# Kernel optimization log

Measured on AMD Instinct MI355X. Metric: run time of the kernel, lower is better.

Reference implementation:

```python
import jax, jax.numpy as jnp
import numpy as np

HIDDEN = 1024
D_INNER = 2048
DT_RANK = 64
STATE = 16
KCONV = 4


def setup_inputs() -> dict:
    key = jax.random.key(0)
    ks = jax.random.split(key, 9)
    s = lambda k, shape, sc=0.02: jax.random.normal(k, shape, dtype=jnp.float32) * sc
    return {
        "x": jax.random.normal(ks[0], (2, 1024, HIDDEN), dtype=jnp.float32),
        "in_proj_w": s(ks[1], (2 * D_INNER, HIDDEN)),
        "conv_w": s(ks[2], (D_INNER, 1, KCONV), 0.2),
        "conv_b": s(ks[3], (D_INNER,), 0.1),
        "x_proj_w": s(ks[4], (DT_RANK + 2 * STATE, D_INNER)),
        "dt_proj_w": s(ks[5], (D_INNER, DT_RANK), 0.1),
        "dt_proj_b": s(ks[6], (D_INNER,), 0.1),
        "A_log": s(ks[7], (D_INNER, STATE), 0.5),
        "out_proj_w": s(ks[8], (HIDDEN, D_INNER)),
    }


def _selective_scan(u, delta, A, B, C):
    # u, delta: (b,l,d); A: (d,n); B, C: (b,l,n)
    deltaA = jnp.exp(delta[..., None] * A)               # (b,l,d,n)
    dBu = (delta * u)[..., None] * B[:, :, None, :]      # (b,l,d,n)
    # scan over time axis; carry h: (b,d,n)
    deltaA_t = jnp.moveaxis(deltaA, 1, 0)                # (l,b,d,n)
    dBu_t = jnp.moveaxis(dBu, 1, 0)                      # (l,b,d,n)
    C_t = jnp.moveaxis(C, 1, 0)                          # (l,b,n)

    def step(h, inp):
        dA_i, dBu_i, C_i = inp
        h = dA_i * h + dBu_i
        y = jnp.einsum('bdn,bn->bd', h, C_i)
        return h, y

    h0 = jnp.zeros(u.shape[:1] + u.shape[2:] + (A.shape[1],), dtype=u.dtype)
    _, ys = jax.lax.scan(step, h0, (deltaA_t, dBu_t, C_t))
    return jnp.moveaxis(ys, 0, 1)                        # (b,l,d)


def reference(x, in_proj_w, conv_w, conv_b, x_proj_w, dt_proj_w, dt_proj_b, A_log, out_proj_w):
    b, l, _ = x.shape
    xr = x @ in_proj_w.T                                 # (b,l,2*d_inner)
    xs, res = jnp.split(xr, 2, axis=-1)
    # causal depthwise conv1d: pad left k-1 (matches padding=k-1 then [:l])
    xc = jnp.moveaxis(xs, 1, 2)                          # (b,d,l)
    xc = jax.lax.conv_general_dilated(
        xc, conv_w, window_strides=(1,), padding=[(KCONV - 1, 0)],
        feature_group_count=D_INNER,
        dimension_numbers=('NCH', 'OIH', 'NCH'))
    xc = xc + conv_b[None, :, None]
    xs = jnp.moveaxis(xc, 2, 1)                          # (b,l,d)
    xs = jax.nn.silu(xs)
    x_dbl = xs @ x_proj_w.T                              # (b,l,dt_rank+2n)
    dt, B, C = jnp.split(x_dbl, [DT_RANK, DT_RANK + STATE], axis=-1)
    delta = jax.nn.softplus(dt @ dt_proj_w.T + dt_proj_b)
    A = -jnp.exp(A_log.astype(jnp.float32))
    y = _selective_scan(xs, delta, A, B, C)
    y = y * jax.nn.silu(res)
    return y @ out_proj_w.T
```

## Files before the change

### kernel.cpp

```cpp
#include <hip/hip_runtime.h>

typedef unsigned short u16;
typedef __bf16 bf16x8 __attribute__((ext_vector_type(8)));
typedef float f32x4 __attribute__((ext_vector_type(4)));

__device__ inline float bf2f(u16 u) {
    unsigned int x = ((unsigned int)u) << 16;
    return __builtin_bit_cast(float, x);
}
__device__ inline u16 f2bf(float f) {
    unsigned int x = __builtin_bit_cast(unsigned int, f);
    return (u16)((x + 0x7FFFu + ((x >> 16) & 1u)) >> 16);
}
__device__ inline float sigm(float v) { return 1.f / (1.f + __expf(-v)); }

__device__ __forceinline__ void gload16(const void* g, void* l) {
    __builtin_amdgcn_global_load_lds(
        (const __attribute__((address_space(1))) void*)g,
        (__attribute__((address_space(3))) void*)l, 16, 0, 0);
}

__device__ inline uint4 pack8(const float* p) {
    const float4* q = (const float4*)p;
    float4 a = q[0], b = q[1];
    union { u16 h[8]; uint4 v; } u;
    u.h[0] = f2bf(a.x); u.h[1] = f2bf(a.y); u.h[2] = f2bf(a.z); u.h[3] = f2bf(a.w);
    u.h[4] = f2bf(b.x); u.h[5] = f2bf(b.y); u.h[6] = f2bf(b.z); u.h[7] = f2bf(b.w);
    return u.v;
}

__global__ __launch_bounds__(256)
void cvt_front(const float* __restrict__ x, const float* __restrict__ inw,
               const float* __restrict__ xpw, const float* __restrict__ convw,
               u16* __restrict__ x_bf, u16* __restrict__ inw_bf,
               u16* __restrict__ xpw_bf, float* __restrict__ wt)
{
    int bk = blockIdx.x, tid = threadIdx.x;
    if (bk < 1024) {
        int i = bk * 256 + tid;
        ((uint4*)x_bf)[i] = pack8(x + (size_t)i * 8);
    } else if (bk < 3072) {
        int i = (bk - 1024) * 256 + tid;
        ((uint4*)inw_bf)[i] = pack8(inw + (size_t)i * 8);
    } else if (bk < 3200) {
        int i = (bk - 3072) * 256 + tid;
        int row = (i * 8) >> 11;
        ((uint4*)xpw_bf)[i] = (row < 96) ? pack8(xpw + (size_t)row * 2048 + ((i * 8) & 2047))
                                         : make_uint4(0u, 0u, 0u, 0u);
    } else {
        int i = (bk - 3200) * 256 + tid;
        wt[(i & 3) * 2048 + (i >> 2)] = convw[i];
    }
}

__global__ __launch_bounds__(256)
void cvt_bf16(const float* __restrict__ in, u16* __restrict__ out)
{
    int i = blockIdx.x * 256 + threadIdx.x;
    ((uint4*)out)[i] = pack8(in + (size_t)i * 8);
}

template<int EPI, bool OUTF32>
__global__ __launch_bounds__(256, 2)
void gemm2(const u16* __restrict__ A, int lda,
           const u16* __restrict__ B, int ldb,
           void* __restrict__ Cout, int ldc,
           int N, int ksplit, size_t zElems,
           const float* __restrict__ bias)
{
    __shared__ u16 sA[128][64];
    __shared__ u16 sB[128][64];

    const int tid  = threadIdx.x;
    const int lane = tid & 63;
    const int wave = tid >> 6;

    int nxy = gridDim.x * gridDim.y;
    int id  = blockIdx.y * gridDim.x + blockIdx.x;
    int bx, by;
    if ((nxy & 7) == 0) {
        int cpx = nxy >> 3;
        int swz = (id & 7) * cpx + (id >> 3);
        bx = swz % gridDim.x;
        by = swz / gridDim.x;
    } else { bx = blockIdx.x; by = blockIdx.y; }

    const int wm = (wave >> 1) * 64;
    const int wn = (wave & 1) * 64;
    const int m0 = by * 128;
    const int n0 = bx * 128;
    const int lm = lane & 15;
    const int g  = lane >> 4;
    const int k0 = blockIdx.z * ksplit;

    const int rr = lane >> 3;
    const int sl = lane & 7;
    const int xsl = sl ^ rr;
    const u16* gA = A + (size_t)(m0 + wave * 8 + rr) * lda + k0 + xsl * 8;
    const u16* gB = B + (size_t)(n0 + wave * 8 + rr) * ldb + k0 + xsl * 8;
    const int ldsRow = (wave * 8) * 128;

    f32x4 acc[4][4] = {};

    for (int kb = 0; kb < ksplit; kb += 64) {
        #pragma unroll
        for (int c = 0; c < 4; ++c) {
            gload16(gA + (size_t)c * 32 * lda + kb, (char*)sA + c * 4096 + ldsRow);
            gload16(gB + (size_t)c * 32 * ldb + kb, (char*)sB + c * 4096 + ldsRow);
        }
        __syncthreads();

        bf16x8 af[2][4], bfr[2][4];
        #pragma unroll
        for (int h = 0; h < 2; ++h) {
            #pragma unroll
            for (int i = 0; i < 4; ++i) {
                int ra = wm + i * 16 + lm;
                int rb = wn + i * 16 + lm;
                int chunk = (((h << 2) | g) ^ (lm & 7)) << 4;
                af[h][i]  = *(const bf16x8*)((const char*)sA + ra * 128 + chunk);
                bfr[h][i] = *(const bf16x8*)((const char*)sB + rb * 128 + chunk);
            }
        }
        #pragma unroll
        for (int h = 0; h < 2; ++h)
            #pragma unroll
            for (int i = 0; i < 4; ++i)
                #pragma unroll
                for (int j = 0; j < 4; ++j)
                    acc[i][j] = __builtin_amdgcn_mfma_f32_16x16x32_bf16(af[h][i], bfr[h][j], acc[i][j], 0, 0, 0);
        __syncthreads();
    }

    #pragma unroll
    for (int i = 0; i < 4; ++i) {
        int crow = m0 + wm + i * 16 + ((lane >> 4) << 2);
        #pragma unroll
        for (int j = 0; j < 4; ++j) {
            int ccol = n0 + wn + j * 16 + lm;
            if (ccol < N) {
                #pragma unroll
                for (int r = 0; r < 4; ++r) {
                    float v = acc[i][j][r];
                    if (EPI == 2 && ccol >= 2048) v *= sigm(v);
                    size_t off = (size_t)blockIdx.z * zElems + (size_t)(crow + r) * ldc + ccol;
                    if (OUTF32) ((float*)Cout)[off] = v;
                    else        ((u16*)Cout)[off]   = f2bf(v);
                }
            }
        }
    }
}

__global__ __launch_bounds__(256)
void dt_delta(const u16* __restrict__ xdbl, const float* __restrict__ dtw,
              const float* __restrict__ bias, u16* __restrict__ out)
{
    const int tid = threadIdx.x;
    const int d   = blockIdx.x * 256 + tid;
    const int t0  = blockIdx.y * 16;

    __shared__ float s_x[16][64];

    if (tid < 128) {
        int tok = tid >> 3, ch = tid & 7;
        uint4 v = *(const uint4*)&xdbl[(size_t)(t0 + tok) * 96 + ch * 8];
        const u16* h = (const u16*)&v;
        #pragma unroll
        for (int e = 0; e < 8; ++e) s_x[tok][ch * 8 + e] = bf2f(h[e]);
    }

    float w[64];
    {
        const float4* wp = (const float4*)(dtw + (size_t)d * 64);
        #pragma unroll
        for (int q = 0; q < 16; ++q) {
            float4 v = wp[q];
            w[q * 4 + 0] = v.x; w[q * 4 + 1] = v.y;
            w[q * 4 + 2] = v.z; w[q * 4 + 3] = v.w;
        }
    }
    const float bd = bias[d];
    __syncthreads();

    for (int tok = 0; tok < 16; ++tok) {
        float a0 = bd, a1 = 0.f, a2 = 0.f, a3 = 0.f;
        const float4* xv4 = (const float4*)s_x[tok];
        #pragma unroll
        for (int q = 0; q < 16; ++q) {
            float4 xv = xv4[q];
            a0 = fmaf(w[q * 4 + 0], xv.x, a0);
            a1 = fmaf(w[q * 4 + 1], xv.y, a1);
            a2 = fmaf(w[q * 4 + 2], xv.z, a2);
            a3 = fmaf(w[q * 4 + 3], xv.w, a3);
        }
        float v = (a0 + a1) + (a2 + a3);
        v = (v > 20.f) ? v : log1pf(__expf(v));
        out[(size_t)(t0 + tok) * 4096 + d] = f2bf(v);
    }
}

__global__ __launch_bounds__(256)
void reduce96(const float* __restrict__ splits, u16* __restrict__ xdbl)
{
    int i = blockIdx.x * 256 + threadIdx.x;
    float acc = 0.f;
    #pragma unroll
    for (int z = 0; z < 8; ++z) acc += splits[(size_t)z * 196608 + i];
    xdbl[i] = f2bf(acc);
}

__global__ __launch_bounds__(256)
void reduce_out(const u16* __restrict__ parts, float* __restrict__ out)
{
    int i = blockIdx.x * 256 + threadIdx.x;
    float acc[8] = {};
    #pragma unroll
    for (int z = 0; z < 4; ++z) {
        uint4 v = ((const uint4*)(parts + (size_t)z * 2097152))[i];
        const u16* h = (const u16*)&v;
        #pragma unroll
        for (int e = 0; e < 8; ++e) acc[e] += bf2f(h[e]);
    }
    float4* o = (float4*)(out + (size_t)i * 8);
    o[0] = make_float4(acc[0], acc[1], acc[2], acc[3]);
    o[1] = make_float4(acc[4], acc[5], acc[6], acc[7]);
}

__global__ __launch_bounds__(256)
void conv_silu(const u16* __restrict__ xr, const float* __restrict__ wt,
               const float* __restrict__ bias, u16* __restrict__ xs)
{
    int gi = blockIdx.x * 256 + threadIdx.x;
    int d  = (gi & 255) * 8;
    int t  = (gi >> 8) & 1023;
    int b  = gi >> 18;
    const u16* base = xr + (size_t)b * 4194304 + d;
    float acc[8];
    {
        const float4* bp = (const float4*)(bias + d);
        float4 b0 = bp[0], b1 = bp[1];
        acc[0]=b0.x; acc[1]=b0.y; acc[2]=b0.z; acc[3]=b0.w;
        acc[4]=b1.x; acc[5]=b1.y; acc[6]=b1.z; acc[7]=b1.w;
    }
    #pragma unroll
    for (int j = 0; j < 4; ++j) {
        int ti = t - 3 + j;
        if (ti >= 0) {
            uint4 v = *(const uint4*)(base + (size_t)ti * 4096);
            const u16* h = (const u16*)&v;
            const float4* wp = (const float4*)(wt + j * 2048 + d);
            float4 w0 = wp[0], w1 = wp[1];
            float w8[8] = {w0.x, w0.y, w0.z, w0.w, w1.x, w1.y, w1.z, w1.w};
            #pragma unroll
            for (int e = 0; e < 8; ++e) acc[e] = fmaf(w8[e], bf2f(h[e]), acc[e]);
        }
    }
    union { u16 h[8]; uint4 v; } o;
    #pragma unroll
    for (int e = 0; e < 8; ++e) { float v = acc[e]; o.h[e] = f2bf(v * sigm(v)); }
    ((uint4*)xs)[gi] = o.v;
}

template<int PHC>
__global__ __launch_bounds__(256)
void scan_chunk(const u16* __restrict__ deltag, u16* __restrict__ xsg,
                const u16* __restrict__ xdbl, const float* __restrict__ A_log,
                const u16* __restrict__ xr, float* __restrict__ summ,
                float* __restrict__ ssum)
{
    const int tid = threadIdx.x;
    const int d0 = blockIdx.x * 256;
    const int c  = blockIdx.y;
    const int b  = blockIdx.z;
    const int d  = d0 + tid;
    const int tok0 = b * 1024 + c * 32;

    __shared__ u16 s_del[32][256];
    __shared__ u16 s_uu[32][256];
    __shared__ u16 s_bc[32][32];
    __shared__ u16 s_res[PHC ? 32 : 1][PHC ? 256 : 1];
    __shared__ u16 s_y[PHC ? 32 : 1][PHC ? 256 : 1];

    for (int i = tid; i < 1024; i += 256) {
        int tl = i >> 5, v = i & 31;
        size_t tok = (size_t)(tok0 + tl);
        *(uint4*)&s_del[tl][v * 8] = *(const uint4*)&deltag[tok * 4096 + d0 + v * 8];
        *(uint4*)&s_uu[tl][v * 8]  = *(const uint4*)&xsg[tok * 2048 + d0 + v * 8];
        if (PHC)
            *(uint4*)&s_res[tl][v * 8] = *(const uint4*)&xr[tok * 4096 + 2048 + d0 + v * 8];
    }
    for (int i = tid; i < 1024; i += 256) {
        int tl = i >> 5, j = i & 31;
        s_bc[tl][j] = xdbl[(size_t)(tok0 + tl) * 96 + 64 + j];
    }

    float Ar[16], h[16];
    {
        const float4* Ap = (const float4*)(A_log + (size_t)d * 16);
        #pragma unroll
        for (int q = 0; q < 4; ++q) {
            float4 a = Ap[q];
            Ar[q * 4 + 0] = -__expf(a.x); Ar[q * 4 + 1] = -__expf(a.y);
            Ar[q * 4 + 2] = -__expf(a.z); Ar[q * 4 + 3] = -__expf(a.w);
        }
    }
    if (PHC) {
        const float4* hp = (const float4*)&summ[((size_t)(b * 32 + c) * 2048 + d) * 16];
        #pragma unroll
        for (int q = 0; q < 4; ++q) {
            float4 v = hp[q];
            h[q * 4 + 0] = v.x; h[q * 4 + 1] = v.y; h[q * 4 + 2] = v.z; h[q * 4 + 3] = v.w;
        }
    } else {
        #pragma unroll
        for (int n = 0; n < 16; ++n) h[n] = 0.f;
    }
    __syncthreads();

    float S = 0.f;
    #pragma unroll 4
    for (int tl = 0; tl < 32; ++tl) {
        float dlt = bf2f(s_del[tl][tid]);
        float du = dlt * bf2f(s_uu[tl][tid]);
        if (!PHC) S += dlt;
        #pragma unroll
        for (int n = 0; n < 16; ++n)
            h[n] = fmaf(__expf(dlt * Ar[n]), h[n], du * bf2f(s_bc[tl][n]));
        if (PHC) {
            float y = 0.f;
            #pragma unroll
            for (int n = 0; n < 16; ++n)
                y = fmaf(h[n], bf2f(s_bc[tl][16 + n]), y);
            s_y[tl][tid] = f2bf(y * bf2f(s_res[tl][tid]));
        }
    }

    if (!PHC) {
        float4* bp = (float4*)&summ[((size_t)(b * 32 + c) * 2048 + d) * 16];
        #pragma unroll
        for (int q = 0; q < 4; ++q)
            bp[q] = make_float4(h[q * 4], h[q * 4 + 1], h[q * 4 + 2], h[q * 4 + 3]);
        ssum[(size_t)(b * 32 + c) * 2048 + d] = S;
    } else {
        __syncthreads();
        for (int i = tid; i < 1024; i += 256) {
            int tl = i >> 5, v = i & 31;
            *(uint4*)&xsg[(size_t)(tok0 + tl) * 2048 + d0 + v * 8] = *(uint4*)&s_y[tl][v * 8];
        }
    }
}

__global__ __launch_bounds__(256)
void scan_phaseB(float* __restrict__ summ, const float* __restrict__ ssum,
                 const float* __restrict__ A_log)
{
    int g = blockIdx.x * 256 + threadIdx.x;
    int n = g & 15;
    int d = (g >> 4) & 2047;
    int b = g >> 15;
    float An = -__expf(A_log[(size_t)d * 16 + n]);
    float h = 0.f;
    for (int c = 0; c < 32; ++c) {
        size_t idx = ((size_t)(b * 32 + c) * 2048 + d) * 16 + n;
        float bc = summ[idx];
        float Sc = ssum[(size_t)(b * 32 + c) * 2048 + d];
        summ[idx] = h;
        h = fmaf(__expf(An * Sc), h, bc);
    }
}

__global__ void sentinel_kernel(float* out, float v) { out[0] = v; }

extern "C" void kernel_launch(void* const* d_in, const int* in_sizes, int n_in,
                              void* d_out, int out_size, void* d_ws, size_t ws_size,
                              hipStream_t stream)
{
    const float* x         = (const float*)d_in[0];
    const float* in_w      = (const float*)d_in[1];
    const float* conv_w    = (const float*)d_in[2];
    const float* conv_b    = (const float*)d_in[3];
    const float* xproj_w   = (const float*)d_in[4];
    const float* dtproj_w  = (const float*)d_in[5];
    const float* dtproj_b  = (const float*)d_in[6];
    const float* A_log     = (const float*)d_in[7];
    const float* outproj_w = (const float*)d_in[8];
    float* out = (float*)d_out;

    static const int EXP[9] = {2097152, 4194304, 8192, 2048, 196608, 131072, 2048, 32768, 2097152};
    int bad = -1;
    if (n_in != 9) bad = 9;
    else { for (int i = 0; i < 9; ++i) if (in_sizes[i] != EXP[i]) { bad = i; break; } }
    if (bad < 0 && out_size != 2097152) bad = 10;
    if (bad < 0 && ws_size < 34734080u) bad = 11;
    if (bad >= 0) {
        sentinel_kernel<<<1, 1, 0, stream>>>(out, 131072.f * (1.f + (float)bad / 16.f));
        return;
    }

    char* ws = (char*)d_ws;
    u16*   xr      = (u16*)(ws);
    u16*   xs      = (u16*)(ws + 16777216);
    u16*   xdbl    = (u16*)(ws + 25165824);
    char*  R       = ws + 25559040;
    u16*   x_bf    = xs;
    u16*   inw_bf  = (u16*)(R);
    u16*   xpw_bf  = (u16*)(R + 8388608);
    float* wt      = (float*)(R + 8912896);
    float* splits  = (float*)(R);
    float* summ    = (float*)(R);
    float* ssum    = (float*)(R + 8388608);
    u16*   opw_bf  = (u16*)(R);
    u16*   oparts  = xr;

    cvt_front<<<3232, 256, 0, stream>>>(x, in_w, xproj_w, conv_w,
                                        x_bf, inw_bf, xpw_bf, wt);
    gemm2<2, false><<<dim3(32, 16, 1), 256, 0, stream>>>(
        x_bf, 1024, inw_bf, 1024, xr, 4096, 4096, 1024, 0, nullptr);
    conv_silu<<<2048, 256, 0, stream>>>(xr, wt, conv_b, xs);
    gemm2<0, true><<<dim3(1, 16, 8), 256, 0, stream>>>(
        xs, 2048, xpw_bf, 2048, splits, 96, 96, 256, 196608, nullptr);
    reduce96<<<768, 256, 0, stream>>>(splits, xdbl);
    dt_delta<<<dim3(8, 128), 256, 0, stream>>>(xdbl, dtproj_w, dtproj_b, xr);
    scan_chunk<0><<<dim3(8, 32, 2), 256, 0, stream>>>(xr, xs, xdbl, A_log, xr, summ, ssum);
    scan_phaseB<<<256, 256, 0, stream>>>(summ, ssum, A_log);
    scan_chunk<1><<<dim3(8, 32, 2), 256, 0, stream>>>(xr, xs, xdbl, A_log, xr, summ, ssum);
    cvt_bf16<<<1024, 256, 0, stream>>>(outproj_w, opw_bf);
    gemm2<0, false><<<dim3(8, 16, 4), 256, 0, stream>>>(
        xs, 2048, opw_bf, 2048, oparts, 1024, 1024, 512, 2097152, nullptr);
    reduce_out<<<1024, 256, 0, stream>>>(oparts, out);
}
```

Measured before the change: 244.6 us.

## Fuse out_proj weight conversion into GEMM, use exp2 in scan, batch phaseB loads

Drops the separate cvt_bf16 launch for the out_proj weights: the GEMM now reads the fp32 B operand directly and packs it to bf16 into LDS itself. The scan kernels fold log2(e) into A and call the raw v_exp_f32 instruction instead of __expf, which saves a multiply per exponential. scan_phaseB loads all 32 chunk summaries into registers up front, so the serial chain no longer waits on scattered loads. In exchange, every GEMM tile that touches a weight block converts it again instead of converting once, and phaseB holds more registers.

```diff
diff --git a/kernel.cpp b/kernel.cpp
--- a/kernel.cpp
+++ b/kernel.cpp
@@ -13,6 +13,9 @@
     return (u16)((x + 0x7FFFu + ((x >> 16) & 1u)) >> 16);
 }
 __device__ inline float sigm(float v) { return 1.f / (1.f + __expf(-v)); }
+__device__ inline float ex2(float x) {
+    float r; asm("v_exp_f32 %0, %1" : "=v"(r) : "v"(x)); return r;
+}
 
 __device__ __forceinline__ void gload16(const void* g, void* l) {
     __builtin_amdgcn_global_load_lds(
@@ -53,17 +56,10 @@
     }
 }
 
-__global__ __launch_bounds__(256)
-void cvt_bf16(const float* __restrict__ in, u16* __restrict__ out)
-{
-    int i = blockIdx.x * 256 + threadIdx.x;
-    ((uint4*)out)[i] = pack8(in + (size_t)i * 8);
-}
-
-template<int EPI, bool OUTF32>
+template<int EPI, bool OUTF32, int BSRC>
 __global__ __launch_bounds__(256, 2)
 void gemm2(const u16* __restrict__ A, int lda,
-           const u16* __restrict__ B, int ldb,
+           const void* __restrict__ Bv, int ldb,
            void* __restrict__ Cout, int ldc,
            int N, int ksplit, size_t zElems,
            const float* __restrict__ bias)
@@ -97,7 +93,8 @@
     const int sl = lane & 7;
     const int xsl = sl ^ rr;
     const u16* gA = A + (size_t)(m0 + wave * 8 + rr) * lda + k0 + xsl * 8;
-    const u16* gB = B + (size_t)(n0 + wave * 8 + rr) * ldb + k0 + xsl * 8;
+    const u16*  gB  = (BSRC == 0) ? (const u16*)Bv + (size_t)(n0 + wave * 8 + rr) * ldb + k0 + xsl * 8 : nullptr;
+    const float* gBf = (BSRC == 1) ? (const float*)Bv + (size_t)(n0 + wave * 8 + rr) * ldb + k0 + xsl * 8 : nullptr;
     const int ldsRow = (wave * 8) * 128;
 
     f32x4 acc[4][4] = {};
@@ -106,7 +103,15 @@
         #pragma unroll
         for (int c = 0; c < 4; ++c) {
             gload16(gA + (size_t)c * 32 * lda + kb, (char*)sA + c * 4096 + ldsRow);
-            gload16(gB + (size_t)c * 32 * ldb + kb, (char*)sB + c * 4096 + ldsRow);
+            if (BSRC == 0)
+                gload16(gB + (size_t)c * 32 * ldb + kb, (char*)sB + c * 4096 + ldsRow);
+        }
+        if (BSRC == 1) {
+            #pragma unroll
+            for (int c = 0; c < 4; ++c) {
+                uint4 v = pack8(gBf + (size_t)c * 32 * ldb + kb);
+                *(uint4*)((char*)sB + c * 4096 + ldsRow + (lane << 4)) = v;
+            }
         }
         __syncthreads();
 
@@ -301,8 +306,10 @@
         #pragma unroll
         for (int q = 0; q < 4; ++q) {
             float4 a = Ap[q];
-            Ar[q * 4 + 0] = -__expf(a.x); Ar[q * 4 + 1] = -__expf(a.y);
-            Ar[q * 4 + 2] = -__expf(a.z); Ar[q * 4 + 3] = -__expf(a.w);
+            Ar[q * 4 + 0] = -__expf(a.x) * 1.44269504f;
+            Ar[q * 4 + 1] = -__expf(a.y) * 1.44269504f;
+            Ar[q * 4 + 2] = -__expf(a.z) * 1.44269504f;
+            Ar[q * 4 + 3] = -__expf(a.w) * 1.44269504f;
         }
     }
     if (PHC) {
@@ -326,7 +333,7 @@
         if (!PHC) S += dlt;
         #pragma unroll
         for (int n = 0; n < 16; ++n)
-            h[n] = fmaf(__expf(dlt * Ar[n]), h[n], du * bf2f(s_bc[tl][n]));
+            h[n] = fmaf(ex2(dlt * Ar[n]), h[n], du * bf2f(s_bc[tl][n]));
         if (PHC) {
             float y = 0.f;
             #pragma unroll
@@ -359,15 +366,22 @@
     int n = g & 15;
     int d = (g >> 4) & 2047;
     int b = g >> 15;
-    float An = -__expf(A_log[(size_t)d * 16 + n]);
+    float An2 = -__expf(A_log[(size_t)d * 16 + n]) * 1.44269504f;
+    size_t base = ((size_t)(b * 32) * 2048 + d) * 16 + n;
+    float bc[32], Sc[32];
+    #pragma unroll
+    for (int c = 0; c < 32; ++c) bc[c] = summ[base + (size_t)c * 32768];
+    #pragma unroll
+    for (int c = 0; c < 32; ++c) Sc[c] = ssum[(size_t)(b * 32 + c) * 2048 + d];
     float h = 0.f;
+    #pragma unroll
     for (int c = 0; c < 32; ++c) {
-        size_t idx = ((size_t)(b * 32 + c) * 2048 + d) * 16 + n;
-        float bc = summ[idx];
-        float Sc = ssum[(size_t)(b * 32 + c) * 2048 + d];
-        summ[idx] = h;
-        h = fmaf(__expf(An * Sc), h, bc);
-    }
+        float nb = bc[c];
+        bc[c] = h;
+        h = fmaf(ex2(An2 * Sc[c]), h, nb);
+    }
+    #pragma unroll
+    for (int c = 0; c < 32; ++c) summ[base + (size_t)c * 32768] = bc[c];
 }
 
 __global__ void sentinel_kernel(float* out, float v) { out[0] = v; }
@@ -410,23 +424,21 @@
     float* splits  = (float*)(R);
     float* summ    = (float*)(R);
     float* ssum    = (float*)(R + 8388608);
-    u16*   opw_bf  = (u16*)(R);
     u16*   oparts  = xr;
 
     cvt_front<<<3232, 256, 0, stream>>>(x, in_w, xproj_w, conv_w,
                                         x_bf, inw_bf, xpw_bf, wt);
-    gemm2<2, false><<<dim3(32, 16, 1), 256, 0, stream>>>(
+    gemm2<2, false, 0><<<dim3(32, 16, 1), 256, 0, stream>>>(
         x_bf, 1024, inw_bf, 1024, xr, 4096, 4096, 1024, 0, nullptr);
     conv_silu<<<2048, 256, 0, stream>>>(xr, wt, conv_b, xs);
-    gemm2<0, true><<<dim3(1, 16, 8), 256, 0, stream>>>(
+    gemm2<0, true, 0><<<dim3(1, 16, 8), 256, 0, stream>>>(
         xs, 2048, xpw_bf, 2048, splits, 96, 96, 256, 196608, nullptr);
     reduce96<<<768, 256, 0, stream>>>(splits, xdbl);
     dt_delta<<<dim3(8, 128), 256, 0, stream>>>(xdbl, dtproj_w, dtproj_b, xr);
     scan_chunk<0><<<dim3(8, 32, 2), 256, 0, stream>>>(xr, xs, xdbl, A_log, xr, summ, ssum);
     scan_phaseB<<<256, 256, 0, stream>>>(summ, ssum, A_log);
     scan_chunk<1><<<dim3(8, 32, 2), 256, 0, stream>>>(xr, xs, xdbl, A_log, xr, summ, ssum);
-    cvt_bf16<<<1024, 256, 0, stream>>>(outproj_w, opw_bf);
-    gemm2<0, false><<<dim3(8, 16, 4), 256, 0, stream>>>(
-        xs, 2048, opw_bf, 2048, oparts, 1024, 1024, 512, 2097152, nullptr);
+    gemm2<0, false, 1><<<dim3(8, 16, 4), 256, 0, stream>>>(
+        xs, 2048, outproj_w, 2048, oparts, 1024, 1024, 512, 2097152, nullptr);
     reduce_out<<<1024, 256, 0, stream>>>(oparts, out);
 }
```

Measured after the change: 250.8 us. +2.6%, slower.
